# Kernel optimization log

Hardware: AMD Instinct MI355X
Metric: run time of the kernel (lower is better)

Reference implementation:

```python
import jax, jax.numpy as jnp
import numpy as np

SEQ_LEN = 720
PRED_LEN = 720
ENC_IN = 862
PCA_RANK = 32
CUT_FREQ = 48
LENGTH_RATIO = (SEQ_LEN + PRED_LEN) / SEQ_LEN  # 2.0
FREQ_OUT = int(CUT_FREQ * LENGTH_RATIO)        # 96
B = 256


def setup_inputs() -> dict:
    key = jax.random.key(0)
    ks = jax.random.split(key, 7)
    return {
        "x_enc": jax.random.normal(ks[0], (B, SEQ_LEN, ENC_IN), dtype=jnp.float32),
        "pca_encode": jax.random.normal(ks[1], (ENC_IN, PCA_RANK), dtype=jnp.float32),
        "pca_decode": jax.random.normal(ks[2], (PCA_RANK, ENC_IN), dtype=jnp.float32),
        "Wr": jax.random.normal(ks[3], (PCA_RANK, FREQ_OUT, CUT_FREQ), dtype=jnp.float32) * 0.1,
        "Wi": jax.random.normal(ks[4], (PCA_RANK, FREQ_OUT, CUT_FREQ), dtype=jnp.float32) * 0.1,
        "br": jax.random.normal(ks[5], (PCA_RANK, FREQ_OUT), dtype=jnp.float32) * 0.1,
        "bi": jax.random.normal(ks[6], (PCA_RANK, FREQ_OUT), dtype=jnp.float32) * 0.1,
    }


def reference(x_enc, pca_encode, pca_decode, Wr, Wi, br, bi):
    # PCA compress: [B, T, C] @ [C, R] -> [B, T, R]
    x = x_enc @ pca_encode
    # Instance normalization over time (torch.var default is unbiased, ddof=1)
    x_mean = x.mean(axis=1, keepdims=True)
    x = x - x_mean
    x_var = jnp.var(x, axis=1, keepdims=True, ddof=1)
    x_std = jnp.sqrt(x_var + 1e-5)
    x = x / x_std
    # Frequency-domain linear, batched over the R channels as one complex GEMM
    x_freq_low = jnp.fft.rfft(x, axis=1)[:, :CUT_FREQ, :]        # [B, F, R] complex
    W = (Wr + 1j * Wi).astype(jnp.complex64)                     # [R, G, F]
    b = (br + 1j * bi).astype(jnp.complex64)                     # [R, G]
    out_freq = jnp.einsum('bfr,rgf->bgr', x_freq_low, W) + b.T[None]  # [B, G, R]
    # Inverse FFT to the extended length, rescale, take prediction horizon
    out = jnp.fft.irfft(out_freq, n=SEQ_LEN + PRED_LEN, axis=1) * LENGTH_RATIO
    out = out[:, -PRED_LEN:, :]
    # De-normalize and PCA decompress
    out = out * x_std + x_mean
    return out @ pca_decode  # [B, pred_len, C]
```

## Files before the change

### kernel.cpp

```cpp
#include <hip/hip_runtime.h>
#include <math.h>

#define B_SZ   256
#define T_SEQ  720
#define C_INN  862
#define RANK   32
#define FCUT   48
#define GOUT   96
#define KTILES 27

#define WMR_OFF    (0)
#define WMI_OFF    (147456)
#define PARTF_OFF  (294912)
#define PARTG_OFF  (2654208)
#define STATSG_OFF (2703360)
#define OBG_OFF    (2719744)
#define PSWZ_OFF   (5898240)
#define FTABB_OFF  (5912064)
#define ITABB_OFF  (5947392)
#define DSWZ_OFF   (6016512)

typedef __attribute__((ext_vector_type(8))) short bf16x8;
typedef __attribute__((ext_vector_type(4))) float f32x4;

__device__ inline short f2bf(float f) {
    union { float f; unsigned u; } v; v.f = f;
    unsigned r = (v.u + 0x7fffu + ((v.u >> 16) & 1u)) >> 16;
    return (short)r;
}
__device__ inline unsigned pkhi(float lo, float hi) {
    return __builtin_amdgcn_perm(__float_as_uint(hi), __float_as_uint(lo), 0x07060302u);
}
union U8 { bf16x8 v; unsigned u[4]; };

__device__ inline int swz_bid(int bid, int chunks_per_xcd) {
    return (bid & 7) * chunks_per_xcd + (bid >> 3);
}

__global__ __launch_bounds__(256) void k_prep(const float* __restrict__ P,
                                              const float* __restrict__ D,
                                              const float* __restrict__ Wr,
                                              const float* __restrict__ Wi,
                                              short* __restrict__ Pswz,
                                              short* __restrict__ ftabB,
                                              short* __restrict__ itabB,
                                              short* __restrict__ Dswz,
                                              float4* __restrict__ WmR,
                                              float4* __restrict__ WmI) {
    int idx = blockIdx.x * 256 + threadIdx.x;
    const float TWO_PI = 6.28318530717958647692f;
    if (idx < 138240) {
        int i = idx & 7, l = (idx >> 3) & 63, rest = idx >> 9;
        int ks = rest % 6, mt = rest / 6;
        int t = mt * 16 + (l & 15);
        int k = ks * 32 + ((l >> 4) << 3) + i;
        int g = k >> 1, odd = k & 1;
        float val;
        if (g == 0) {
            val = odd ? 0.0f : 0.5f;
        } else {
            int m = (g * (720 + t)) % 1440;
            float th = TWO_PI * (float)m * (1.0f / 1440.0f);
            val = odd ? sinf(th) : cosf(th);
        }
        itabB[idx] = f2bf(val);
    } else if (idx < 138240 + 70656) {
        int j = idx - 138240;
        int i = j & 7, l = (j >> 3) & 63, rest = j >> 9;
        int ks = rest % 23, mt = rest / 23;
        int row = mt * 16 + (l & 15);
        int t = ks * 32 + ((l >> 4) << 3) + i;
        int f = row >> 1, odd = row & 1;
        float val = 0.0f;
        if (t < T_SEQ) {
            int m = (f * t) % T_SEQ;
            float th = TWO_PI * (float)m * (1.0f / 720.0f);
            val = odd ? -sinf(th) : cosf(th);
        }
        ftabB[j] = f2bf(val);
    } else if (idx < 138240 + 70656 + 27648) {
        int j = idx - 138240 - 70656;
        int i = j & 7, lane = (j >> 3) & 63, rest = j >> 9;
        int ct = rest & 1, kt = rest >> 1;
        int k = kt * 32 + ((lane >> 4) << 3) + i;
        int c = ct * 16 + (lane & 15);
        float v = (k < C_INN) ? P[k * RANK + c] : 0.0f;
        Pswz[j] = f2bf(v);
    } else if (idx < 264192) {
        int j = idx - 138240 - 70656 - 27648;
        int i = j & 7, lane = (j >> 3) & 63, ct = j >> 9;
        int k = ((lane >> 4) << 3) + i;
        int c = ct * 16 + (lane & 15);
        float v = (c < C_INN) ? D[k * C_INN + c] : 0.0f;
        Dswz[j] = f2bf(v);
    } else {
        int j = idx - 264192;
        int r = j & 31;
        int q = (j >> 5) % 12;
        int g = (j >> 5) / 12;
        size_t src = ((size_t)(r * 96 + g)) * 48 + q * 4;
        WmR[(g * 12 + q) * 32 + r] = *(const float4*)(Wr + src);
        WmI[(g * 12 + q) * 32 + r] = *(const float4*)(Wi + src);
    }
}

__global__ __launch_bounds__(512) void k_encode(const float* __restrict__ x,
                                                const short* __restrict__ Pswz,
                                                const short* __restrict__ ftabB,
                                                float* __restrict__ partF,
                                                float* __restrict__ partg) {
    __shared__ short YbL[8192];
    __shared__ float red[512];
    int bid = swz_bid(blockIdx.x, 96);
    int b = bid / 3, seg = bid % 3;
    int tid = threadIdx.x, l = tid & 63, w = tid >> 6;
    int h = l >> 4, c0 = l & 15, c1 = c0 + 16;
    const float* xb = x + (size_t)b * T_SEQ * C_INN;
    const bf16x8* pb = (const bf16x8*)Pswz;

    int mtbase = seg * 16;
    int ksbase = seg * 8;
    int nks    = (seg < 2) ? 8 : 7;
    int mt0 = mtbase + w;
    int mt1 = mtbase + 8 + w;
    bool valid1 = (seg < 2) || (w < 5);
    const float* xr0 = xb + (size_t)(mt0 * 16 + c0) * C_INN;
    const float* xr1 = valid1 ? (xb + (size_t)(mt1 * 16 + c0) * C_INN) : xr0;

    if (seg == 2 && tid < 128) {
        int ct = tid >> 6;
        int lp = 32 + ((tid >> 1) & 31);
        int half = tid & 1;
        short4 z; z.x = 0; z.y = 0; z.z = 0; z.w = 0;
        *(short4*)&YbL[((6 * 2 + ct) * 64 + lp) * 8 + half * 4] = z;
    }

    f32x4 acc00 = {0,0,0,0}, acc01 = {0,0,0,0};
    f32x4 acc10 = {0,0,0,0}, acc11 = {0,0,0,0};

#pragma unroll 2
    for (int kt = 0; kt < KTILES - 1; ++kt) {
        int kbase = kt * 32 + h * 8;
        float4 u00 = *(const float4*)(xr0 + kbase);
        float4 u01 = *(const float4*)(xr0 + kbase + 4);
        float4 u10 = *(const float4*)(xr1 + kbase);
        float4 u11 = *(const float4*)(xr1 + kbase + 4);
        bf16x8 b0 = pb[(kt * 2 + 0) * 64 + l];
        bf16x8 b1 = pb[(kt * 2 + 1) * 64 + l];
        U8 A0, A1;
        A0.u[0] = pkhi(u00.x, u00.y); A0.u[1] = pkhi(u00.z, u00.w);
        A0.u[2] = pkhi(u01.x, u01.y); A0.u[3] = pkhi(u01.z, u01.w);
        A1.u[0] = pkhi(u10.x, u10.y); A1.u[1] = pkhi(u10.z, u10.w);
        A1.u[2] = pkhi(u11.x, u11.y); A1.u[3] = pkhi(u11.z, u11.w);
        acc00 = __builtin_amdgcn_mfma_f32_16x16x32_bf16(A0.v, b0, acc00, 0, 0, 0);
        acc01 = __builtin_amdgcn_mfma_f32_16x16x32_bf16(A0.v, b1, acc01, 0, 0, 0);
        acc10 = __builtin_amdgcn_mfma_f32_16x16x32_bf16(A1.v, b0, acc10, 0, 0, 0);
        acc11 = __builtin_amdgcn_mfma_f32_16x16x32_bf16(A1.v, b1, acc11, 0, 0, 0);
    }
    {
        int kbase = 832 + h * 8;
        bf16x8 b0 = pb[(26 * 2 + 0) * 64 + l];
        bf16x8 b1 = pb[(26 * 2 + 1) * 64 + l];
        const float* xrs[2] = {xr0, xr1};
        f32x4* accs[2][2] = {{&acc00,&acc01},{&acc10,&acc11}};
#pragma unroll
        for (int tt = 0; tt < 2; ++tt) {
            const float* xr = xrs[tt];
            float vals[8];
            float2 u0 = *(const float2*)(xr + kbase);
            float2 u1 = *(const float2*)(xr + kbase + 2);
            float2 u2 = *(const float2*)(xr + kbase + 4);
            vals[0] = u0.x; vals[1] = u0.y;
            vals[2] = u1.x; vals[3] = u1.y;
            vals[4] = u2.x; vals[5] = u2.y;
            if (h < 3) {
                float2 u3 = *(const float2*)(xr + kbase + 6);
                vals[6] = u3.x; vals[7] = u3.y;
            } else {
                vals[6] = 0.f; vals[7] = 0.f;
            }
            U8 A;
            A.u[0] = pkhi(vals[0], vals[1]); A.u[1] = pkhi(vals[2], vals[3]);
            A.u[2] = pkhi(vals[4], vals[5]); A.u[3] = pkhi(vals[6], vals[7]);
            *accs[tt][0] = __builtin_amdgcn_mfma_f32_16x16x32_bf16(A.v, b0, *accs[tt][0], 0, 0, 0);
            *accs[tt][1] = __builtin_amdgcn_mfma_f32_16x16x32_bf16(A.v, b1, *accs[tt][1], 0, 0, 0);
        }
    }

    {
        float s0 = 0.f, q0 = 0.f, s1 = 0.f, q1 = 0.f;
#pragma unroll
        for (int j = 0; j < 4; ++j) {
            float v;
            v = acc00[j]; s0 += v; q0 += v * v;
            v = acc01[j]; s1 += v; q1 += v * v;
            if (valid1) {
                v = acc10[j]; s0 += v; q0 += v * v;
                v = acc11[j]; s1 += v; q1 += v * v;
            }
        }
        s0 += __shfl_xor(s0, 16); s0 += __shfl_xor(s0, 32);
        q0 += __shfl_xor(q0, 16); q0 += __shfl_xor(q0, 32);
        s1 += __shfl_xor(s1, 16); s1 += __shfl_xor(s1, 32);
        q1 += __shfl_xor(q1, 16); q1 += __shfl_xor(q1, 32);
        if (l < 16) {
            red[c0 * 8 + w]       = s0;
            red[c1 * 8 + w]       = s1;
            red[256 + c0 * 8 + w] = q0;
            red[256 + c1 * 8 + w] = q1;
        }
    }
    __syncthreads();
    if (tid < 32) {
        float s = 0.f;
        for (int ww = 0; ww < 8; ++ww) s += red[tid * 8 + ww];
        partg[bid * 64 + tid] = s;
    } else if (tid < 64) {
        int c = tid - 32;
        float q = 0.f;
        for (int ww = 0; ww < 8; ++ww) q += red[256 + c * 8 + ww];
        partg[bid * 64 + tid] = q;
    }

    {
        int ibase = (h & 1) * 4;
#define WRTILEL(MT, A0v, A1v)                                                      \
        {                                                                          \
            int lp  = ((2 * (MT) + (h >> 1)) & 3) * 16 + c0;                       \
            int ksl = ((MT) >> 1) - ksbase;                                        \
            short4 w0, w1;                                                         \
            w0.x = f2bf(A0v[0]); w0.y = f2bf(A0v[1]);                              \
            w0.z = f2bf(A0v[2]); w0.w = f2bf(A0v[3]);                              \
            w1.x = f2bf(A1v[0]); w1.y = f2bf(A1v[1]);                              \
            w1.z = f2bf(A1v[2]); w1.w = f2bf(A1v[3]);                              \
            *(short4*)&YbL[((ksl * 2 + 0) * 64 + lp) * 8 + ibase] = w0;            \
            *(short4*)&YbL[((ksl * 2 + 1) * 64 + lp) * 8 + ibase] = w1;            \
        }
        WRTILEL(mt0, acc00, acc01);
        if (valid1) WRTILEL(mt1, acc10, acc11);
#undef WRTILEL
    }
    __syncthreads();

    {
        float* pf = partF + (size_t)bid * 3072;
        for (int idx = w; idx < 12; idx += 8) {
            int fmt = idx >> 1, fct = idx & 1;
            f32x4 acc = {0.f, 0.f, 0.f, 0.f};
            for (int ksl = 0; ksl < nks; ++ksl) {
                bf16x8 a  = ((const bf16x8*)ftabB)[(fmt * 23 + ksbase + ksl) * 64 + l];
                bf16x8 bb = *(const bf16x8*)&YbL[((ksl * 2 + fct) * 64 + l) * 8];
                acc = __builtin_amdgcn_mfma_f32_16x16x32_bf16(a, bb, acc, 0, 0, 0);
            }
#pragma unroll
            for (int j = 0; j < 4; ++j)
                pf[(fmt * 16 + h * 4 + j) * 32 + fct * 16 + c0] = acc[j];
        }
    }
}

__global__ __launch_bounds__(512) void k_front(const float* __restrict__ partF,
                                               const float* __restrict__ partg,
                                               float* __restrict__ statsg,
                                               const float4* __restrict__ WmR,
                                               const float4* __restrict__ WmI,
                                               const float* __restrict__ brr,
                                               const float* __restrict__ bii,
                                               short* __restrict__ OBg) {
    __shared__ float Fre[FCUT * 32];
    __shared__ float Fim[FCUT * 32];
    __shared__ float meanS[32], istdS[32];
    int b   = blockIdx.x;
    int tid = threadIdx.x;

    if (tid < 32) {
        const float* pg = partg + (size_t)b * 192;
        float s = pg[tid] + pg[64 + tid] + pg[128 + tid];
        float q = pg[32 + tid] + pg[96 + tid] + pg[160 + tid];
        float mean = s / 720.0f;
        float var  = (q - 720.0f * mean * mean) / 719.0f;
        float sd   = sqrtf(var + 1e-5f);
        meanS[tid] = mean;
        istdS[tid] = 1.0f / sd;
        statsg[b * 64 + tid]      = mean;
        statsg[b * 64 + 32 + tid] = sd;
    }
    __syncthreads();

    {
        const float* p0 = partF + (size_t)b * 3 * 3072;
        for (int e = tid; e < 3072; e += 512) {
            int row = e >> 5, r = e & 31;
            float v = p0[e] + p0[3072 + e] + p0[6144 + e];
            if (row == 0) v -= 720.0f * meanS[r];
            v *= istdS[r];
            int f = row >> 1;
            if (row & 1) Fim[f * 32 + r] = v;
            else         Fre[f * 32 + r] = v;
        }
    }
    __syncthreads();

    {
        int r = tid & 31, gg = tid >> 5;
        unsigned* OBb = (unsigned*)(OBg + (size_t)b * 6144);
        for (int g = gg; g < GOUT; g += 16) {
            float are = brr[r * GOUT + g];
            float aim = bii[r * GOUT + g];
            const float4* wr4 = WmR + (size_t)g * 384 + r;
            const float4* wi4 = WmI + (size_t)g * 384 + r;
#pragma unroll 3
            for (int q = 0; q < 12; ++q) {
                float4 wr = wr4[q * 32], wi = wi4[q * 32];
                int f0 = q * 4;
                float fr, fi;
                fr = Fre[(f0 + 0) * 32 + r]; fi = Fim[(f0 + 0) * 32 + r];
                are += fr * wr.x - fi * wi.x;  aim += fr * wi.x + fi * wr.x;
                fr = Fre[(f0 + 1) * 32 + r]; fi = Fim[(f0 + 1) * 32 + r];
                are += fr * wr.y - fi * wi.y;  aim += fr * wi.y + fi * wr.y;
                fr = Fre[(f0 + 2) * 32 + r]; fi = Fim[(f0 + 2) * 32 + r];
                are += fr * wr.z - fi * wi.z;  aim += fr * wi.z + fi * wr.z;
                fr = Fre[(f0 + 3) * 32 + r]; fi = Fim[(f0 + 3) * 32 + r];
                are += fr * wr.w - fi * wi.w;  aim += fr * wi.w + fi * wr.w;
            }
            int ks   = g >> 4;
            int kk   = (2 * g) & 31;
            int lane = (kk >> 3) * 16 + (r & 15);
            int ct   = r >> 4;
            unsigned lo = (unsigned short)f2bf(are);
            unsigned hi = (unsigned short)f2bf(-aim);
            OBb[((((ks * 2 + ct) * 64 + lane) * 8) + (kk & 7)) >> 1] = lo | (hi << 16);
        }
    }
}

__global__ __launch_bounds__(512) void k_dec(const short* __restrict__ OBg,
                                             const float* __restrict__ statsg,
                                             const short* __restrict__ itabB,
                                             const short* __restrict__ Dswz,
                                             float* __restrict__ out) {
    __shared__ short zfrag[15 * 512];
    __shared__ __align__(16) float stage[16 * 862];
    int bid = swz_bid(blockIdx.x, 96);
    int b = bid / 3, seg = bid % 3;
    int tid = threadIdx.x, l = tid & 63, w = tid >> 6;
    int h = l >> 4, c0 = l & 15, c1 = c0 + 16;
    const bf16x8* ob = (const bf16x8*)(OBg + (size_t)b * 6144);
    const bf16x8* db = (const bf16x8*)Dswz;
    float* outb = out + (size_t)b * T_SEQ * C_INN;

    float mu0 = statsg[b * 64 + c0], sd0 = statsg[b * 64 + 32 + c0];
    float mu1 = statsg[b * 64 + c1], sd1 = statsg[b * 64 + 32 + c1];

    int lp0 = (c0 >> 3) * 16 + h * 4;
    int lp1 = (2 + (c0 >> 3)) * 16 + h * 4;

    for (int ti = w; ti < 15; ti += 8) {
        int mt = seg * 15 + ti;
        f32x4 A0 = {0.f, 0.f, 0.f, 0.f};
        f32x4 A1 = {0.f, 0.f, 0.f, 0.f};
#pragma unroll
        for (int ks = 0; ks < 6; ++ks) {
            bf16x8 a  = ((const bf16x8*)itabB)[(mt * 6 + ks) * 64 + l];
            bf16x8 b0 = ob[(ks * 2 + 0) * 64 + l];
            bf16x8 b1 = ob[(ks * 2 + 1) * 64 + l];
            A0 = __builtin_amdgcn_mfma_f32_16x16x32_bf16(a, b0, A0, 0, 0, 0);
            A1 = __builtin_amdgcn_mfma_f32_16x16x32_bf16(a, b1, A1, 0, 0, 0);
        }
        short* zf = zfrag + ti * 512;
#pragma unroll
        for (int j = 0; j < 4; ++j) {
            zf[(lp0 + j) * 8 + (l & 7)] = f2bf(A0[j] * (1.0f / 360.0f) * sd0 + mu0);
            zf[(lp1 + j) * 8 + (l & 7)] = f2bf(A1[j] * (1.0f / 360.0f) * sd1 + mu1);
        }
    }
    __syncthreads();

    for (int ti = 0; ti < 15; ++ti) {
        int mt = seg * 15 + ti;
        bf16x8 a = *(const bf16x8*)&zfrag[ti * 512 + l * 8];
        for (int ct = w; ct < 54; ct += 8) {
            bf16x8 bb = db[ct * 64 + l];
            f32x4 acc = {0.f, 0.f, 0.f, 0.f};
            acc = __builtin_amdgcn_mfma_f32_16x16x32_bf16(a, bb, acc, 0, 0, 0);
            int c = ct * 16 + c0;
            if (c < C_INN) {
#pragma unroll
                for (int j = 0; j < 4; ++j)
                    stage[(h * 4 + j) * C_INN + c] = acc[j];
            }
        }
        __syncthreads();
        float* dst = outb + (size_t)mt * 16 * C_INN;
        const f32x4* sg4 = (const f32x4*)stage;
        for (int f = tid; f < 3448; f += 512)
            __builtin_nontemporal_store(sg4[f], (f32x4*)(dst + f * 4));
        __syncthreads();
    }
}

extern "C" void kernel_launch(void* const* d_in, const int* in_sizes, int n_in,
                              void* d_out, int out_size, void* d_ws, size_t ws_size,
                              hipStream_t stream) {
    const float* x   = (const float*)d_in[0];
    const float* P   = (const float*)d_in[1];
    const float* D   = (const float*)d_in[2];
    const float* Wr  = (const float*)d_in[3];
    const float* Wi  = (const float*)d_in[4];
    const float* brr = (const float*)d_in[5];
    const float* bii = (const float*)d_in[6];
    float* out = (float*)d_out;
    float* ws  = (float*)d_ws;

    float4* WmR   = (float4*)(ws + WMR_OFF);
    float4* WmI   = (float4*)(ws + WMI_OFF);
    float*  partF = ws + PARTF_OFF;
    float*  partg = ws + PARTG_OFF;
    float*  statsg= ws + STATSG_OFF;
    short*  OBg   = (short*)(ws + OBG_OFF);
    short*  Pswz  = (short*)(ws + PSWZ_OFF);
    short*  ftabB = (short*)(ws + FTABB_OFF);
    short*  itabB = (short*)(ws + ITABB_OFF);
    short*  Dswz  = (short*)(ws + DSWZ_OFF);

    k_prep<<<1176, 256, 0, stream>>>(P, D, Wr, Wi, Pswz, ftabB, itabB, Dswz, WmR, WmI);
    k_encode<<<768, 512, 0, stream>>>(x, Pswz, ftabB, partF, partg);
    k_front<<<B_SZ, 512, 0, stream>>>(partF, partg, statsg, WmR, WmI, brr, bii, OBg);
    k_dec<<<768, 512, 0, stream>>>(OBg, statsg, itabB, Dswz, out);
}
```

Before: 316.2 us.

## Fuse front stage into encode via last-block atomic counter; nontemporal x loads

Removes the separate k_front launch. Each of the three segment blocks per batch bumps an atomic counter after a threadfence, and the last one to finish runs the stats, normalization and frequency-linear stage, reusing its shared memory. The counter is zeroed in k_prep. The main x loads in the encode loop also become nontemporal so the streaming input does not pollute cache. The gain is one fewer launch and a shorter tail, at the cost of serialized front work on a subset of blocks and reliance on correct fence ordering.

```diff
diff --git a/kernel.cpp b/kernel.cpp
--- a/kernel.cpp
+++ b/kernel.cpp
@@ -19,6 +19,7 @@
 #define FTABB_OFF  (5912064)
 #define ITABB_OFF  (5947392)
 #define DSWZ_OFF   (6016512)
+#define CNT_OFF    (6030336)
 
 typedef __attribute__((ext_vector_type(8))) short bf16x8;
 typedef __attribute__((ext_vector_type(4))) float f32x4;
@@ -32,6 +33,10 @@
     return __builtin_amdgcn_perm(__float_as_uint(hi), __float_as_uint(lo), 0x07060302u);
 }
 union U8 { bf16x8 v; unsigned u[4]; };
+
+__device__ inline f32x4 ntl4(const float* p) {
+    return __builtin_nontemporal_load((const f32x4*)p);
+}
 
 __device__ inline int swz_bid(int bid, int chunks_per_xcd) {
     return (bid & 7) * chunks_per_xcd + (bid >> 3);
@@ -46,7 +51,9 @@
                                               short* __restrict__ itabB,
                                               short* __restrict__ Dswz,
                                               float4* __restrict__ WmR,
-                                              float4* __restrict__ WmI) {
+                                              float4* __restrict__ WmI,
+                                              int* __restrict__ cnt) {
+    if (blockIdx.x == 0) cnt[threadIdx.x] = 0;
     int idx = blockIdx.x * 256 + threadIdx.x;
     const float TWO_PI = 6.28318530717958647692f;
     if (idx < 138240) {
@@ -93,7 +100,7 @@
         int c = ct * 16 + (lane & 15);
         float v = (c < C_INN) ? D[k * C_INN + c] : 0.0f;
         Dswz[j] = f2bf(v);
-    } else {
+    } else if (idx < 301056) {
         int j = idx - 264192;
         int r = j & 31;
         int q = (j >> 5) % 12;
@@ -107,10 +114,18 @@
 __global__ __launch_bounds__(512) void k_encode(const float* __restrict__ x,
                                                 const short* __restrict__ Pswz,
                                                 const short* __restrict__ ftabB,
+                                                const float4* __restrict__ WmR,
+                                                const float4* __restrict__ WmI,
+                                                const float* __restrict__ brr,
+                                                const float* __restrict__ bii,
                                                 float* __restrict__ partF,
-                                                float* __restrict__ partg) {
+                                                float* __restrict__ partg,
+                                                float* __restrict__ statsg,
+                                                short* __restrict__ OBg,
+                                                int* __restrict__ cnt) {
     __shared__ short YbL[8192];
     __shared__ float red[512];
+    __shared__ int lastFlag;
     int bid = swz_bid(blockIdx.x, 96);
     int b = bid / 3, seg = bid % 3;
     int tid = threadIdx.x, l = tid & 63, w = tid >> 6;
@@ -141,17 +156,17 @@
 #pragma unroll 2
     for (int kt = 0; kt < KTILES - 1; ++kt) {
         int kbase = kt * 32 + h * 8;
-        float4 u00 = *(const float4*)(xr0 + kbase);
-        float4 u01 = *(const float4*)(xr0 + kbase + 4);
-        float4 u10 = *(const float4*)(xr1 + kbase);
-        float4 u11 = *(const float4*)(xr1 + kbase + 4);
+        f32x4 u00 = ntl4(xr0 + kbase);
+        f32x4 u01 = ntl4(xr0 + kbase + 4);
+        f32x4 u10 = ntl4(xr1 + kbase);
+        f32x4 u11 = ntl4(xr1 + kbase + 4);
         bf16x8 b0 = pb[(kt * 2 + 0) * 64 + l];
         bf16x8 b1 = pb[(kt * 2 + 1) * 64 + l];
         U8 A0, A1;
-        A0.u[0] = pkhi(u00.x, u00.y); A0.u[1] = pkhi(u00.z, u00.w);
-        A0.u[2] = pkhi(u01.x, u01.y); A0.u[3] = pkhi(u01.z, u01.w);
-        A1.u[0] = pkhi(u10.x, u10.y); A1.u[1] = pkhi(u10.z, u10.w);
-        A1.u[2] = pkhi(u11.x, u11.y); A1.u[3] = pkhi(u11.z, u11.w);
+        A0.u[0] = pkhi(u00[0], u00[1]); A0.u[1] = pkhi(u00[2], u00[3]);
+        A0.u[2] = pkhi(u01[0], u01[1]); A0.u[3] = pkhi(u01[2], u01[3]);
+        A1.u[0] = pkhi(u10[0], u10[1]); A1.u[1] = pkhi(u10[2], u10[3]);
+        A1.u[2] = pkhi(u11[0], u11[1]); A1.u[3] = pkhi(u11[2], u11[3]);
         acc00 = __builtin_amdgcn_mfma_f32_16x16x32_bf16(A0.v, b0, acc00, 0, 0, 0);
         acc01 = __builtin_amdgcn_mfma_f32_16x16x32_bf16(A0.v, b1, acc01, 0, 0, 0);
         acc10 = __builtin_amdgcn_mfma_f32_16x16x32_bf16(A1.v, b0, acc10, 0, 0, 0);
@@ -257,21 +272,21 @@
                 pf[(fmt * 16 + h * 4 + j) * 32 + fct * 16 + c0] = acc[j];
         }
     }
-}
-
-__global__ __launch_bounds__(512) void k_front(const float* __restrict__ partF,
-                                               const float* __restrict__ partg,
-                                               float* __restrict__ statsg,
-                                               const float4* __restrict__ WmR,
-                                               const float4* __restrict__ WmI,
-                                               const float* __restrict__ brr,
-                                               const float* __restrict__ bii,
-                                               short* __restrict__ OBg) {
-    __shared__ float Fre[FCUT * 32];
-    __shared__ float Fim[FCUT * 32];
-    __shared__ float meanS[32], istdS[32];
-    int b   = blockIdx.x;
-    int tid = threadIdx.x;
+
+    __threadfence();
+    __syncthreads();
+    if (tid == 0) {
+        int old = atomicAdd(&cnt[b], 1);
+        lastFlag = (old == 2);
+    }
+    __syncthreads();
+    if (!lastFlag) return;
+    __threadfence();
+
+    float* FreL  = (float*)YbL;
+    float* FimL  = (float*)((char*)YbL + 6144);
+    float* meanL = (float*)((char*)YbL + 12288);
+    float* istdL = (float*)((char*)YbL + 12416);
 
     if (tid < 32) {
         const float* pg = partg + (size_t)b * 192;
@@ -280,8 +295,8 @@
         float mean = s / 720.0f;
         float var  = (q - 720.0f * mean * mean) / 719.0f;
         float sd   = sqrtf(var + 1e-5f);
-        meanS[tid] = mean;
-        istdS[tid] = 1.0f / sd;
+        meanL[tid] = mean;
+        istdL[tid] = 1.0f / sd;
         statsg[b * 64 + tid]      = mean;
         statsg[b * 64 + 32 + tid] = sd;
     }
@@ -292,11 +307,11 @@
         for (int e = tid; e < 3072; e += 512) {
             int row = e >> 5, r = e & 31;
             float v = p0[e] + p0[3072 + e] + p0[6144 + e];
-            if (row == 0) v -= 720.0f * meanS[r];
-            v *= istdS[r];
+            if (row == 0) v -= 720.0f * meanL[r];
+            v *= istdL[r];
             int f = row >> 1;
-            if (row & 1) Fim[f * 32 + r] = v;
-            else         Fre[f * 32 + r] = v;
+            if (row & 1) FimL[f * 32 + r] = v;
+            else         FreL[f * 32 + r] = v;
         }
     }
     __syncthreads();
@@ -314,13 +329,13 @@
                 float4 wr = wr4[q * 32], wi = wi4[q * 32];
                 int f0 = q * 4;
                 float fr, fi;
-                fr = Fre[(f0 + 0) * 32 + r]; fi = Fim[(f0 + 0) * 32 + r];
+                fr = FreL[(f0 + 0) * 32 + r]; fi = FimL[(f0 + 0) * 32 + r];
                 are += fr * wr.x - fi * wi.x;  aim += fr * wi.x + fi * wr.x;
-                fr = Fre[(f0 + 1) * 32 + r]; fi = Fim[(f0 + 1) * 32 + r];
+                fr = FreL[(f0 + 1) * 32 + r]; fi = FimL[(f0 + 1) * 32 + r];
                 are += fr * wr.y - fi * wi.y;  aim += fr * wi.y + fi * wr.y;
-                fr = Fre[(f0 + 2) * 32 + r]; fi = Fim[(f0 + 2) * 32 + r];
+                fr = FreL[(f0 + 2) * 32 + r]; fi = FimL[(f0 + 2) * 32 + r];
                 are += fr * wr.z - fi * wi.z;  aim += fr * wi.z + fi * wr.z;
-                fr = Fre[(f0 + 3) * 32 + r]; fi = Fim[(f0 + 3) * 32 + r];
+                fr = FreL[(f0 + 3) * 32 + r]; fi = FimL[(f0 + 3) * 32 + r];
                 are += fr * wr.w - fi * wi.w;  aim += fr * wi.w + fi * wr.w;
             }
             int ks   = g >> 4;
@@ -422,9 +437,10 @@
     short*  ftabB = (short*)(ws + FTABB_OFF);
     short*  itabB = (short*)(ws + ITABB_OFF);
     short*  Dswz  = (short*)(ws + DSWZ_OFF);
-
-    k_prep<<<1176, 256, 0, stream>>>(P, D, Wr, Wi, Pswz, ftabB, itabB, Dswz, WmR, WmI);
-    k_encode<<<768, 512, 0, stream>>>(x, Pswz, ftabB, partF, partg);
-    k_front<<<B_SZ, 512, 0, stream>>>(partF, partg, statsg, WmR, WmI, brr, bii, OBg);
+    int*    cnt   = (int*)(ws + CNT_OFF);
+
+    k_prep<<<1176, 256, 0, stream>>>(P, D, Wr, Wi, Pswz, ftabB, itabB, Dswz, WmR, WmI, cnt);
+    k_encode<<<768, 512, 0, stream>>>(x, Pswz, ftabB, WmR, WmI, brr, bii,
+                                      partF, partg, statsg, OBg, cnt);
     k_dec<<<768, 512, 0, stream>>>(OBg, statsg, itabB, Dswz, out);
 }
```

After: 839.0 us. 2.65x slower.
